# Kernel optimization log

Measured on AMD Instinct MI355X. Metric: run time of the kernel, lower is better.

## Reference

```python
import jax, jax.numpy as jnp
import numpy as np

LOG2 = 0.6931471805599453

def logcosh(x):
    # numerically stable log(cosh(x)) = |x| + log1p(exp(-2|x|)) - log(2)
    ax = jnp.abs(x)
    return ax + jnp.log1p(jnp.exp(-2.0 * ax)) - LOG2

def setup_inputs() -> dict:
    key = jax.random.key(0)
    k1, k2, k3 = jax.random.split(key, 3)
    B, N, G, F = 16384, 1024, 256, 16  # batch, n_sites, n_symm, alpha_symm
    # each row of perms is a valid permutation of [0, N)
    perms = jax.vmap(lambda k: jax.random.permutation(k, N))(jax.random.split(k1, G)).astype(jnp.int32)
    x = jax.random.normal(k2, (B, N), dtype=jnp.float32)
    W = jax.random.normal(k3, (N, F), dtype=jnp.float32) * 0.1  # kernel_init = normal(0.1)
    b = jnp.zeros((F,), dtype=jnp.float32)
    v_bias = jnp.zeros((1,), dtype=jnp.float32)
    return {"x": x, "W": W, "b": b, "v_bias": v_bias, "perms": perms}

def reference(x, W, b, v_bias, perms):
    # scan over group permutations: gather x by perm, matmul, bias, logcosh, sum
    def f(carry, perm):
        y = x[..., perm] @ W + b          # [B, F]
        return carry + jnp.sum(logcosh(y), axis=-1), None
    y0 = jnp.zeros(x.shape[:-1], dtype=x.dtype)
    y_out, _ = jax.lax.scan(f, y0, perms)
    y_out = y_out + v_bias[0] * jnp.sum(x, axis=-1)
    return y_out
```

## Files before the change

kernel.cpp:

```cpp
#include <hip/hip_runtime.h>
#include <math.h>

typedef __bf16 bf16x8 __attribute__((ext_vector_type(8)));
typedef float f32x4 __attribute__((ext_vector_type(4)));


__device__ __forceinline__ unsigned short f2bf(float f) {
    unsigned int u = __float_as_uint(f);
    u += 0x7FFFu + ((u >> 16) & 1u);
    return (unsigned short)(u >> 16);
}

__device__ __forceinline__ float logcosh_fast(float v) {
    float a = fabsf(v);
    float t = __expf(-2.0f * a);
    return a + (__logf(1.0f + t) - 0.6931471805599453f);
}

template <int CTRL>
__device__ __forceinline__ float dppadd(float x) {
    int y = __builtin_amdgcn_update_dpp(0, __float_as_int(x), CTRL, 0xf, 0xf, true);
    return x + __int_as_float(y);
}

__device__ __forceinline__ void gload_lds16(const void* g, void* l) {
    __builtin_amdgcn_global_load_lds(
        (__attribute__((address_space(1))) void*)(void*)g,
        (__attribute__((address_space(3))) void*)l, 16, 0, 0);
}

#define SBAR()  __builtin_amdgcn_s_barrier()
#define SCHED() __builtin_amdgcn_sched_barrier(0)

__global__ __launch_bounds__(256) void k_invert(const int* __restrict__ perms,
                                                int* __restrict__ inv) {
    int t = blockIdx.x * 256 + threadIdx.x;
    int g = t >> 10, n = t & 1023;
    inv[(g << 10) + perms[t]] = n;
}

__global__ __launch_bounds__(256) void k_build_bt(const float* __restrict__ W,
                                                  const int* __restrict__ inv,
                                                  unsigned short* __restrict__ bT) {
    int j = blockIdx.x;
    int g = j >> 4, f = j & 15;
    const int* invg = inv + (g << 10);
    size_t rowbase = (size_t)j << 10;
#pragma unroll
    for (int i = 0; i < 4; ++i) {
        int k = (i << 8) + threadIdx.x;
        int n = invg[k];
        bT[rowbase + k] = f2bf(W[(n << 4) + f]);
    }
}

__global__ __launch_bounds__(256) void k_convert(const float* __restrict__ x,
                                                 const float* __restrict__ vb,
                                                 unsigned short* __restrict__ xb,
                                                 float* __restrict__ out) {
    int row = blockIdx.x, tid = threadIdx.x;
    size_t base = ((size_t)row << 10) + (tid << 2);
    float4 v = *reinterpret_cast<const float4*>(x + base);
    ushort4 h;
    h.x = f2bf(v.x); h.y = f2bf(v.y); h.z = f2bf(v.z); h.w = f2bf(v.w);
    *reinterpret_cast<ushort4*>(xb + base) = h;
    float s = v.x + v.y + v.z + v.w;
#pragma unroll
    for (int off = 32; off > 0; off >>= 1) s += __shfl_down(s, off);
    __shared__ float ls[4];
    if ((tid & 63) == 0) ls[tid >> 6] = s;
    __syncthreads();
    if (tid == 0) out[row] = vb[0] * (ls[0] + ls[1] + ls[2] + ls[3]);
}


#define MFMA_M(MM)                                                               \
    _Pragma("unroll") for (int k_ = 0; k_ < 2; ++k_)                             \
    _Pragma("unroll") for (int n_ = 0; n_ < 4; ++n_)                             \
        acc[MM][n_] = __builtin_amdgcn_mfma_f32_16x16x32_bf16(                   \
            aF[MM][k_], bF[n_][k_], acc[MM][n_], 0, 0, 0);

__device__ __forceinline__ void stage_half(unsigned short* dst,
                                           const unsigned short* src, int h,
                                           int tid, int wv) {
#pragma unroll
    for (int j = 0; j < 2; ++j) {
        int c0 = (h * 128 + j * 64) * 8;
        int cc = c0 + tid;
        int r = cc >> 3;
        int cs = (cc & 7) ^ (r & 7);
        gload_lds16(src + (((size_t)r) << 10) + (cs << 3),
                    dst + ((c0 + wv * 64) << 3));
    }
}

template <bool STAGE, int VM>
__device__ __forceinline__ void tile_iter(
    const unsigned short* Ap, const unsigned short* Bp,
    unsigned short* AsD, unsigned short* BsD,
    const unsigned short* xsrc, const unsigned short* bsrc,
    f32x4 (&acc)[8][4], int aRow, int bRow, int po0, int po1, int tid, int wv) {
    bf16x8 aF[8][2], bF[4][2];

#pragma unroll
    for (int n = 0; n < 4; ++n) {
        bF[n][0] = *reinterpret_cast<const bf16x8*>(Bp + bRow + po0 + n * 1024);
        bF[n][1] = *reinterpret_cast<const bf16x8*>(Bp + bRow + po1 + n * 1024);
    }
#pragma unroll
    for (int m = 0; m < 2; ++m) {
        aF[m][0] = *reinterpret_cast<const bf16x8*>(Ap + aRow + po0 + m * 1024);
        aF[m][1] = *reinterpret_cast<const bf16x8*>(Ap + aRow + po1 + m * 1024);
    }
    SCHED();

#pragma unroll
    for (int m = 0; m < 6; ++m) {
        aF[m + 2][0] = *reinterpret_cast<const bf16x8*>(Ap + aRow + po0 + (m + 2) * 1024);
        aF[m + 2][1] = *reinterpret_cast<const bf16x8*>(Ap + aRow + po1 + (m + 2) * 1024);
        SCHED();
        asm volatile("s_waitcnt lgkmcnt(4)" ::: "memory");
        SCHED();
        __builtin_amdgcn_s_setprio(1);
        MFMA_M(m)
        __builtin_amdgcn_s_setprio(0);
        SCHED();
    }

    asm volatile("s_waitcnt lgkmcnt(0)" ::: "memory");
    SCHED();
    SBAR();

    if (STAGE) { stage_half(AsD, xsrc, 0, tid, wv); stage_half(AsD, xsrc, 1, tid, wv); }
    SCHED();
    __builtin_amdgcn_s_setprio(1);
    MFMA_M(6)
    __builtin_amdgcn_s_setprio(0);
    SCHED();

    if (STAGE) { stage_half(BsD, bsrc, 0, tid, wv); stage_half(BsD, bsrc, 1, tid, wv); }
    SCHED();
    __builtin_amdgcn_s_setprio(1);
    MFMA_M(7)
    __builtin_amdgcn_s_setprio(0);
    SCHED();
    if (VM == 8)      { asm volatile("s_waitcnt vmcnt(8)" ::: "memory"); }
    else if (VM == 0) { asm volatile("s_waitcnt vmcnt(0)" ::: "memory"); }
    SCHED();
    SBAR();
}

__global__ __launch_bounds__(512, 2) void k_gemm(const unsigned short* __restrict__ xb,
                                                 const unsigned short* __restrict__ bT,
                                                 const float* __restrict__ bias,
                                                 float* __restrict__ partial, int B) {
    __shared__ unsigned short As[2][256 * 64];
    __shared__ unsigned short Bs[2][256 * 64];

    const int tid = threadIdx.x;
    const int lane = tid & 63;
    const int wv = tid >> 6;
    const int wm = wv >> 2;
    const int wn = wv & 3;
    const int lr = lane & 15;
    const int lk = lane >> 4;

    const int fid = blockIdx.y * gridDim.x + blockIdx.x;
    const int cpx = (gridDim.x * gridDim.y) >> 3;
    const int swz = (fid & 7) * cpx + (fid >> 3);
    const int cbx = swz & 15;
    const int row0 = (swz >> 4) << 8;
    const int j0 = cbx << 8;

    const unsigned short* xbase = xb + ((size_t)row0 << 10);
    const unsigned short* bbase = bT + ((size_t)j0 << 10);

    const int aRow = (wm * 128 + lr) * 64;
    const int bRow = (wn * 64 + lr) * 64;
    const int po0 = (lk ^ (lr & 7)) * 8;
    const int po1 = ((4 + lk) ^ (lr & 7)) * 8;

    f32x4 acc[8][4];
#pragma unroll
    for (int m = 0; m < 8; ++m)
#pragma unroll
        for (int n = 0; n < 4; ++n)
            acc[m][n] = {0.f, 0.f, 0.f, 0.f};

    stage_half(&As[0][0], xbase, 0, tid, wv);
    stage_half(&As[0][0], xbase, 1, tid, wv);
    stage_half(&Bs[0][0], bbase, 0, tid, wv);
    stage_half(&Bs[0][0], bbase, 1, tid, wv);
    stage_half(&As[1][0], xbase + 64, 0, tid, wv);
    stage_half(&As[1][0], xbase + 64, 1, tid, wv);
    stage_half(&Bs[1][0], bbase + 64, 0, tid, wv);
    stage_half(&Bs[1][0], bbase + 64, 1, tid, wv);
    asm volatile("s_waitcnt vmcnt(8)" ::: "memory");
    SCHED();
    SBAR();

    for (int tt = 0; tt < 7; ++tt) {
        const int t0 = tt * 2;
        tile_iter<true, 8>(&As[0][0], &Bs[0][0], &As[0][0], &Bs[0][0],
                           xbase + ((t0 + 2) << 6), bbase + ((t0 + 2) << 6),
                           acc, aRow, bRow, po0, po1, tid, wv);
        tile_iter<true, 8>(&As[1][0], &Bs[1][0], &As[1][0], &Bs[1][0],
                           xbase + ((t0 + 3) << 6), bbase + ((t0 + 3) << 6),
                           acc, aRow, bRow, po0, po1, tid, wv);
    }
    tile_iter<false, 0>(&As[0][0], &Bs[0][0], &As[0][0], &Bs[0][0],
                        xbase, bbase, acc, aRow, bRow, po0, po1, tid, wv);
    tile_iter<false, -1>(&As[1][0], &Bs[1][0], &As[1][0], &Bs[1][0],
                         xbase, bbase, acc, aRow, bRow, po0, po1, tid, wv);

    float* rowsum = (float*)&As[0][0];
    const float bv = bias[lr];
#pragma unroll
    for (int m = 0; m < 8; ++m) {
#pragma unroll
        for (int r = 0; r < 4; ++r) {
            float s = 0.f;
#pragma unroll
            for (int n = 0; n < 4; ++n) s += logcosh_fast(acc[m][n][r] + bv);
            s = dppadd<0x111>(s);
            s = dppadd<0x112>(s);
            s = dppadd<0x114>(s);
            s = dppadd<0x118>(s);
            if (lr == 15)
                rowsum[wn * 256 + wm * 128 + m * 16 + lk * 4 + r] = s;
        }
    }
    __syncthreads();
    if (tid < 256) {
        float s = rowsum[tid] + rowsum[256 + tid] + rowsum[512 + tid] + rowsum[768 + tid];
        partial[(size_t)cbx * B + row0 + tid] = s;
    }
}

__global__ __launch_bounds__(256) void k_final(const float* __restrict__ partial,
                                               float* __restrict__ out, int ncb, int B) {
    int b = blockIdx.x * 256 + threadIdx.x;
    float s = out[b];
    for (int c = 0; c < ncb; ++c) s += partial[(size_t)c * B + b];
    out[b] = s;
}

extern "C" void kernel_launch(void* const* d_in, const int* in_sizes, int n_in,
                              void* d_out, int out_size, void* d_ws, size_t ws_size,
                              hipStream_t stream) {
    const float* x      = (const float*)d_in[0];
    const float* W      = (const float*)d_in[1];
    const float* bias   = (const float*)d_in[2];
    const float* v_bias = (const float*)d_in[3];
    const int*   perms  = (const int*)d_in[4];
    float* out = (float*)d_out;

    const int N  = 1024;
    const int B  = in_sizes[0] / N;
    const int G  = in_sizes[4] / N;
    const int GF = G * 16;
    const int NCB = GF / 256;

    char* w = (char*)d_ws;
    unsigned short* xb = (unsigned short*)w;
    unsigned short* bT = (unsigned short*)(w + (size_t)B * N * 2);
    int* inv = (int*)(w + (size_t)B * N * 2 + (size_t)GF * N * 2);
    float* partial = (float*)(w + (size_t)B * N * 2 + (size_t)GF * N * 2
                              + (size_t)G * N * 4);

    k_invert<<<G * N / 256, 256, 0, stream>>>(perms, inv);
    k_build_bt<<<GF, 256, 0, stream>>>(W, inv, bT);
    k_convert<<<B, 256, 0, stream>>>(x, v_bias, xb, out);
    k_gemm<<<dim3(NCB, B / 256), 512, 0, stream>>>(xb, bT, bias, partial, B);
    k_final<<<B / 256, 256, 0, stream>>>(partial, out, NCB, B);
}
```

Before: 188.4 us.

## Load B fragments directly to registers and drop LDS staging for B

```diff
diff --git a/kernel.cpp b/kernel.cpp
--- a/kernel.cpp
+++ b/kernel.cpp
@@ -74,77 +74,74 @@
 }
 
 
-#define MFMA_M(MM)                                                               \
-    _Pragma("unroll") for (int k_ = 0; k_ < 2; ++k_)                             \
+#define MFMA_M(MM, AFR)                                                          \
+    _Pragma("unroll") for (int kk_ = 0; kk_ < 2; ++kk_)                          \
     _Pragma("unroll") for (int n_ = 0; n_ < 4; ++n_)                             \
         acc[MM][n_] = __builtin_amdgcn_mfma_f32_16x16x32_bf16(                   \
-            aF[MM][k_], bF[n_][k_], acc[MM][n_], 0, 0, 0);
-
-__device__ __forceinline__ void stage_half(unsigned short* dst,
-                                           const unsigned short* src, int h,
-                                           int tid, int wv) {
-#pragma unroll
-    for (int j = 0; j < 2; ++j) {
-        int c0 = (h * 128 + j * 64) * 8;
-        int cc = c0 + tid;
-        int r = cc >> 3;
-        int cs = (cc & 7) ^ (r & 7);
-        gload_lds16(src + (((size_t)r) << 10) + (cs << 3),
-                    dst + ((c0 + wv * 64) << 3));
-    }
-}
-
-template <bool STAGE, int VM>
-__device__ __forceinline__ void tile_iter(
-    const unsigned short* Ap, const unsigned short* Bp,
-    unsigned short* AsD, unsigned short* BsD,
-    const unsigned short* xsrc, const unsigned short* bsrc,
-    f32x4 (&acc)[8][4], int aRow, int bRow, int po0, int po1, int tid, int wv) {
-    bf16x8 aF[8][2], bF[4][2];
-
-#pragma unroll
-    for (int n = 0; n < 4; ++n) {
-        bF[n][0] = *reinterpret_cast<const bf16x8*>(Bp + bRow + po0 + n * 1024);
-        bF[n][1] = *reinterpret_cast<const bf16x8*>(Bp + bRow + po1 + n * 1024);
-    }
+            AFR[kk_], bF[n_][kk_], acc[MM][n_], 0, 0, 0);
+
+__device__ __forceinline__ void stage_i(unsigned short* dst, const unsigned short* src,
+                                        int voff, int i, int wv) {
+    gload_lds16(src + voff, dst + (((i << 9) + wv * 64) << 3));
+}
+
+template <bool STA, bool LDB, int VM>
+__device__ __forceinline__ void tile_mw(
+    const unsigned short* Ap,
+    unsigned short* Adst,
+    const unsigned short* xsrc,
+    const unsigned short* bcol,
+    int ktN,
+    bf16x8 (&bF)[4][2],
+    f32x4 (&acc)[8][4],
+    const int (&vs)[4], int aRow, int po0, int po1, int wv) {
+    bf16x8 aF[4][2];
+
 #pragma unroll
     for (int m = 0; m < 2; ++m) {
         aF[m][0] = *reinterpret_cast<const bf16x8*>(Ap + aRow + po0 + m * 1024);
         aF[m][1] = *reinterpret_cast<const bf16x8*>(Ap + aRow + po1 + m * 1024);
     }
     SCHED();
-
 #pragma unroll
     for (int m = 0; m < 6; ++m) {
-        aF[m + 2][0] = *reinterpret_cast<const bf16x8*>(Ap + aRow + po0 + (m + 2) * 1024);
-        aF[m + 2][1] = *reinterpret_cast<const bf16x8*>(Ap + aRow + po1 + (m + 2) * 1024);
+        aF[(m + 2) & 3][0] = *reinterpret_cast<const bf16x8*>(Ap + aRow + po0 + (m + 2) * 1024);
+        aF[(m + 2) & 3][1] = *reinterpret_cast<const bf16x8*>(Ap + aRow + po1 + (m + 2) * 1024);
         SCHED();
         asm volatile("s_waitcnt lgkmcnt(4)" ::: "memory");
         SCHED();
         __builtin_amdgcn_s_setprio(1);
-        MFMA_M(m)
+        MFMA_M(m, aF[m & 3])
         __builtin_amdgcn_s_setprio(0);
         SCHED();
     }
-
     asm volatile("s_waitcnt lgkmcnt(0)" ::: "memory");
     SCHED();
     SBAR();
 
-    if (STAGE) { stage_half(AsD, xsrc, 0, tid, wv); stage_half(AsD, xsrc, 1, tid, wv); }
+    if (STA) {
+#pragma unroll
+        for (int i = 0; i < 4; ++i) stage_i(Adst, xsrc, vs[i], i, wv);
+    }
     SCHED();
     __builtin_amdgcn_s_setprio(1);
-    MFMA_M(6)
+    MFMA_M(6, aF[2])
     __builtin_amdgcn_s_setprio(0);
     SCHED();
 
-    if (STAGE) { stage_half(BsD, bsrc, 0, tid, wv); stage_half(BsD, bsrc, 1, tid, wv); }
-    SCHED();
     __builtin_amdgcn_s_setprio(1);
-    MFMA_M(7)
+    MFMA_M(7, aF[3])
     __builtin_amdgcn_s_setprio(0);
     SCHED();
-    if (VM == 8)      { asm volatile("s_waitcnt vmcnt(8)" ::: "memory"); }
+    if (LDB) {
+#pragma unroll
+        for (int n = 0; n < 4; ++n) {
+            bF[n][0] = *reinterpret_cast<const bf16x8*>(bcol + ktN + n * 16384);
+            bF[n][1] = *reinterpret_cast<const bf16x8*>(bcol + ktN + n * 16384 + 32);
+        }
+    }
+    SCHED();
+    if (VM == 12)     { asm volatile("s_waitcnt vmcnt(12)" ::: "memory"); }
     else if (VM == 0) { asm volatile("s_waitcnt vmcnt(0)" ::: "memory"); }
     SCHED();
     SBAR();
@@ -155,7 +152,6 @@
                                                  const float* __restrict__ bias,
                                                  float* __restrict__ partial, int B) {
     __shared__ unsigned short As[2][256 * 64];
-    __shared__ unsigned short Bs[2][256 * 64];
 
     const int tid = threadIdx.x;
     const int lane = tid & 63;
@@ -168,18 +164,27 @@
     const int fid = blockIdx.y * gridDim.x + blockIdx.x;
     const int cpx = (gridDim.x * gridDim.y) >> 3;
     const int swz = (fid & 7) * cpx + (fid >> 3);
-    const int cbx = swz & 15;
-    const int row0 = (swz >> 4) << 8;
+    const int rowb = swz & 63;
+    const int cbx = swz >> 6;
+    const int row0 = rowb << 8;
     const int j0 = cbx << 8;
 
     const unsigned short* xbase = xb + ((size_t)row0 << 10);
-    const unsigned short* bbase = bT + ((size_t)j0 << 10);
+    const unsigned short* bcol = bT + (((size_t)(j0 + wn * 64 + lr)) << 10) + lk * 8;
 
     const int aRow = (wm * 128 + lr) * 64;
-    const int bRow = (wn * 64 + lr) * 64;
     const int po0 = (lk ^ (lr & 7)) * 8;
     const int po1 = ((4 + lk) ^ (lr & 7)) * 8;
 
+    int vs[4];
+#pragma unroll
+    for (int i = 0; i < 4; ++i) {
+        int cc = (i << 9) + tid;
+        int r = cc >> 3;
+        int cs = (cc & 7) ^ (r & 7);
+        vs[i] = (r << 10) + (cs << 3);
+    }
+
     f32x4 acc[8][4];
 #pragma unroll
     for (int m = 0; m < 8; ++m)
@@ -187,31 +192,39 @@
         for (int n = 0; n < 4; ++n)
             acc[m][n] = {0.f, 0.f, 0.f, 0.f};
 
-    stage_half(&As[0][0], xbase, 0, tid, wv);
-    stage_half(&As[0][0], xbase, 1, tid, wv);
-    stage_half(&Bs[0][0], bbase, 0, tid, wv);
-    stage_half(&Bs[0][0], bbase, 1, tid, wv);
-    stage_half(&As[1][0], xbase + 64, 0, tid, wv);
-    stage_half(&As[1][0], xbase + 64, 1, tid, wv);
-    stage_half(&Bs[1][0], bbase + 64, 0, tid, wv);
-    stage_half(&Bs[1][0], bbase + 64, 1, tid, wv);
-    asm volatile("s_waitcnt vmcnt(8)" ::: "memory");
+    bf16x8 bF0[4][2], bF1[4][2];
+
+#pragma unroll
+    for (int i = 0; i < 4; ++i) stage_i(&As[0][0], xbase, vs[i], i, wv);
+#pragma unroll
+    for (int n = 0; n < 4; ++n) {
+        bF0[n][0] = *reinterpret_cast<const bf16x8*>(bcol + n * 16384);
+        bF0[n][1] = *reinterpret_cast<const bf16x8*>(bcol + n * 16384 + 32);
+    }
+#pragma unroll
+    for (int i = 0; i < 4; ++i) stage_i(&As[1][0], xbase + 64, vs[i], i, wv);
+#pragma unroll
+    for (int n = 0; n < 4; ++n) {
+        bF1[n][0] = *reinterpret_cast<const bf16x8*>(bcol + 64 + n * 16384);
+        bF1[n][1] = *reinterpret_cast<const bf16x8*>(bcol + 64 + n * 16384 + 32);
+    }
+    asm volatile("s_waitcnt vmcnt(12)" ::: "memory");
     SCHED();
     SBAR();
 
     for (int tt = 0; tt < 7; ++tt) {
         const int t0 = tt * 2;
-        tile_iter<true, 8>(&As[0][0], &Bs[0][0], &As[0][0], &Bs[0][0],
-                           xbase + ((t0 + 2) << 6), bbase + ((t0 + 2) << 6),
-                           acc, aRow, bRow, po0, po1, tid, wv);
-        tile_iter<true, 8>(&As[1][0], &Bs[1][0], &As[1][0], &Bs[1][0],
-                           xbase + ((t0 + 3) << 6), bbase + ((t0 + 3) << 6),
-                           acc, aRow, bRow, po0, po1, tid, wv);
-    }
-    tile_iter<false, 0>(&As[0][0], &Bs[0][0], &As[0][0], &Bs[0][0],
-                        xbase, bbase, acc, aRow, bRow, po0, po1, tid, wv);
-    tile_iter<false, -1>(&As[1][0], &Bs[1][0], &As[1][0], &Bs[1][0],
-                         xbase, bbase, acc, aRow, bRow, po0, po1, tid, wv);
+        tile_mw<true, true, 12>(&As[0][0], &As[0][0], xbase + ((t0 + 2) << 6),
+                                bcol, (t0 + 2) << 6,
+                                bF0, acc, vs, aRow, po0, po1, wv);
+        tile_mw<true, true, 12>(&As[1][0], &As[1][0], xbase + ((t0 + 3) << 6),
+                                bcol, (t0 + 3) << 6,
+                                bF1, acc, vs, aRow, po0, po1, wv);
+    }
+    tile_mw<false, false, 0>(&As[0][0], &As[0][0], xbase, bcol, 0,
+                             bF0, acc, vs, aRow, po0, po1, wv);
+    tile_mw<false, false, -1>(&As[1][0], &As[1][0], xbase, bcol, 0,
+                              bF1, acc, vs, aRow, po0, po1, wv);
 
     float* rowsum = (float*)&As[0][0];
     const float bv = bias[lr];
```

Result: slower. 246.1 us (+30.6%).

## Shrink GEMM block tile to 128x128 with 256 threads and higher occupancy

Applied to the files above, without the earlier changes.

```diff
diff --git a/kernel.cpp b/kernel.cpp
--- a/kernel.cpp
+++ b/kernel.cpp
@@ -75,32 +75,24 @@
 
 
 #define MFMA_M(MM)                                                               \
-    _Pragma("unroll") for (int k_ = 0; k_ < 2; ++k_)                             \
+    _Pragma("unroll") for (int kk_ = 0; kk_ < 2; ++kk_)                          \
     _Pragma("unroll") for (int n_ = 0; n_ < 4; ++n_)                             \
         acc[MM][n_] = __builtin_amdgcn_mfma_f32_16x16x32_bf16(                   \
-            aF[MM][k_], bF[n_][k_], acc[MM][n_], 0, 0, 0);
-
-__device__ __forceinline__ void stage_half(unsigned short* dst,
-                                           const unsigned short* src, int h,
-                                           int tid, int wv) {
-#pragma unroll
-    for (int j = 0; j < 2; ++j) {
-        int c0 = (h * 128 + j * 64) * 8;
-        int cc = c0 + tid;
-        int r = cc >> 3;
-        int cs = (cc & 7) ^ (r & 7);
-        gload_lds16(src + (((size_t)r) << 10) + (cs << 3),
-                    dst + ((c0 + wv * 64) << 3));
-    }
-}
-
-template <bool STAGE, int VM>
-__device__ __forceinline__ void tile_iter(
+            aF[MM][kk_], bF[n_][kk_], acc[MM][n_], 0, 0, 0);
+
+__device__ __forceinline__ void stage128(unsigned short* dst, const unsigned short* src,
+                                         int voff, int i, int wv) {
+    gload_lds16(src + voff, dst + (((i << 8) + (wv << 6)) << 3));
+}
+
+template <bool ST, int VM>
+__device__ __forceinline__ void tile128(
     const unsigned short* Ap, const unsigned short* Bp,
-    unsigned short* AsD, unsigned short* BsD,
+    unsigned short* Adst, unsigned short* Bdst,
     const unsigned short* xsrc, const unsigned short* bsrc,
-    f32x4 (&acc)[8][4], int aRow, int bRow, int po0, int po1, int tid, int wv) {
-    bf16x8 aF[8][2], bF[4][2];
+    f32x4 (&acc)[4][4], const int (&vs)[4],
+    int aRow, int bRow, int po0, int po1, int wv) {
+    bf16x8 aF[4][2], bF[4][2];
 
 #pragma unroll
     for (int n = 0; n < 4; ++n) {
@@ -113,36 +105,44 @@
         aF[m][1] = *reinterpret_cast<const bf16x8*>(Ap + aRow + po1 + m * 1024);
     }
     SCHED();
-
-#pragma unroll
-    for (int m = 0; m < 6; ++m) {
-        aF[m + 2][0] = *reinterpret_cast<const bf16x8*>(Ap + aRow + po0 + (m + 2) * 1024);
-        aF[m + 2][1] = *reinterpret_cast<const bf16x8*>(Ap + aRow + po1 + (m + 2) * 1024);
-        SCHED();
-        asm volatile("s_waitcnt lgkmcnt(4)" ::: "memory");
-        SCHED();
-        __builtin_amdgcn_s_setprio(1);
-        MFMA_M(m)
-        __builtin_amdgcn_s_setprio(0);
-        SCHED();
-    }
-
+    aF[2][0] = *reinterpret_cast<const bf16x8*>(Ap + aRow + po0 + 2 * 1024);
+    aF[2][1] = *reinterpret_cast<const bf16x8*>(Ap + aRow + po1 + 2 * 1024);
+    SCHED();
+    asm volatile("s_waitcnt lgkmcnt(4)" ::: "memory");
+    SCHED();
+    __builtin_amdgcn_s_setprio(1);
+    MFMA_M(0)
+    __builtin_amdgcn_s_setprio(0);
+    SCHED();
+    aF[3][0] = *reinterpret_cast<const bf16x8*>(Ap + aRow + po0 + 3 * 1024);
+    aF[3][1] = *reinterpret_cast<const bf16x8*>(Ap + aRow + po1 + 3 * 1024);
+    SCHED();
+    asm volatile("s_waitcnt lgkmcnt(4)" ::: "memory");
+    SCHED();
+    __builtin_amdgcn_s_setprio(1);
+    MFMA_M(1)
+    __builtin_amdgcn_s_setprio(0);
+    SCHED();
+    asm volatile("s_waitcnt lgkmcnt(2)" ::: "memory");
+    SCHED();
+    __builtin_amdgcn_s_setprio(1);
+    MFMA_M(2)
+    __builtin_amdgcn_s_setprio(0);
+    SCHED();
     asm volatile("s_waitcnt lgkmcnt(0)" ::: "memory");
     SCHED();
+    __builtin_amdgcn_s_setprio(1);
+    MFMA_M(3)
+    __builtin_amdgcn_s_setprio(0);
+    SCHED();
     SBAR();
 
-    if (STAGE) { stage_half(AsD, xsrc, 0, tid, wv); stage_half(AsD, xsrc, 1, tid, wv); }
-    SCHED();
-    __builtin_amdgcn_s_setprio(1);
-    MFMA_M(6)
-    __builtin_amdgcn_s_setprio(0);
-    SCHED();
-
-    if (STAGE) { stage_half(BsD, bsrc, 0, tid, wv); stage_half(BsD, bsrc, 1, tid, wv); }
-    SCHED();
-    __builtin_amdgcn_s_setprio(1);
-    MFMA_M(7)
-    __builtin_amdgcn_s_setprio(0);
+    if (ST) {
+#pragma unroll
+        for (int i = 0; i < 4; ++i) stage128(Adst, xsrc, vs[i], i, wv);
+#pragma unroll
+        for (int i = 0; i < 4; ++i) stage128(Bdst, bsrc, vs[i], i, wv);
+    }
     SCHED();
     if (VM == 8)      { asm volatile("s_waitcnt vmcnt(8)" ::: "memory"); }
     else if (VM == 0) { asm volatile("s_waitcnt vmcnt(0)" ::: "memory"); }
@@ -150,73 +150,83 @@
     SBAR();
 }
 
-__global__ __launch_bounds__(512, 2) void k_gemm(const unsigned short* __restrict__ xb,
+__global__ __launch_bounds__(256, 4) void k_gemm(const unsigned short* __restrict__ xb,
                                                  const unsigned short* __restrict__ bT,
                                                  const float* __restrict__ bias,
                                                  float* __restrict__ partial, int B) {
-    __shared__ unsigned short As[2][256 * 64];
-    __shared__ unsigned short Bs[2][256 * 64];
+    __shared__ unsigned short As[2][128 * 64];
+    __shared__ unsigned short Bs[2][128 * 64];
 
     const int tid = threadIdx.x;
     const int lane = tid & 63;
     const int wv = tid >> 6;
-    const int wm = wv >> 2;
-    const int wn = wv & 3;
+    const int wm = wv >> 1;
+    const int wn = wv & 1;
     const int lr = lane & 15;
     const int lk = lane >> 4;
 
     const int fid = blockIdx.y * gridDim.x + blockIdx.x;
     const int cpx = (gridDim.x * gridDim.y) >> 3;
     const int swz = (fid & 7) * cpx + (fid >> 3);
-    const int cbx = swz & 15;
-    const int row0 = (swz >> 4) << 8;
-    const int j0 = cbx << 8;
+    const int rowb = swz & 127;
+    const int cbx = swz >> 7;
+    const int row0 = rowb << 7;
+    const int j0 = cbx << 7;
 
     const unsigned short* xbase = xb + ((size_t)row0 << 10);
     const unsigned short* bbase = bT + ((size_t)j0 << 10);
 
-    const int aRow = (wm * 128 + lr) * 64;
+    const int aRow = (wm * 64 + lr) * 64;
     const int bRow = (wn * 64 + lr) * 64;
     const int po0 = (lk ^ (lr & 7)) * 8;
     const int po1 = ((4 + lk) ^ (lr & 7)) * 8;
 
-    f32x4 acc[8][4];
-#pragma unroll
-    for (int m = 0; m < 8; ++m)
+    int vs[4];
+#pragma unroll
+    for (int i = 0; i < 4; ++i) {
+        int cc = (i << 8) + tid;
+        int r = cc >> 3;
+        int cs = (cc & 7) ^ (r & 7);
+        vs[i] = (r << 10) + (cs << 3);
+    }
+
+    f32x4 acc[4][4];
+#pragma unroll
+    for (int m = 0; m < 4; ++m)
 #pragma unroll
         for (int n = 0; n < 4; ++n)
             acc[m][n] = {0.f, 0.f, 0.f, 0.f};
 
-    stage_half(&As[0][0], xbase, 0, tid, wv);
-    stage_half(&As[0][0], xbase, 1, tid, wv);
-    stage_half(&Bs[0][0], bbase, 0, tid, wv);
-    stage_half(&Bs[0][0], bbase, 1, tid, wv);
-    stage_half(&As[1][0], xbase + 64, 0, tid, wv);
-    stage_half(&As[1][0], xbase + 64, 1, tid, wv);
-    stage_half(&Bs[1][0], bbase + 64, 0, tid, wv);
-    stage_half(&Bs[1][0], bbase + 64, 1, tid, wv);
+#pragma unroll
+    for (int i = 0; i < 4; ++i) stage128(&As[0][0], xbase, vs[i], i, wv);
+#pragma unroll
+    for (int i = 0; i < 4; ++i) stage128(&Bs[0][0], bbase, vs[i], i, wv);
+#pragma unroll
+    for (int i = 0; i < 4; ++i) stage128(&As[1][0], xbase + 64, vs[i], i, wv);
+#pragma unroll
+    for (int i = 0; i < 4; ++i) stage128(&Bs[1][0], bbase + 64, vs[i], i, wv);
     asm volatile("s_waitcnt vmcnt(8)" ::: "memory");
     SCHED();
     SBAR();
 
     for (int tt = 0; tt < 7; ++tt) {
         const int t0 = tt * 2;
-        tile_iter<true, 8>(&As[0][0], &Bs[0][0], &As[0][0], &Bs[0][0],
-                           xbase + ((t0 + 2) << 6), bbase + ((t0 + 2) << 6),
-                           acc, aRow, bRow, po0, po1, tid, wv);
-        tile_iter<true, 8>(&As[1][0], &Bs[1][0], &As[1][0], &Bs[1][0],
-                           xbase + ((t0 + 3) << 6), bbase + ((t0 + 3) << 6),
-                           acc, aRow, bRow, po0, po1, tid, wv);
-    }
-    tile_iter<false, 0>(&As[0][0], &Bs[0][0], &As[0][0], &Bs[0][0],
-                        xbase, bbase, acc, aRow, bRow, po0, po1, tid, wv);
-    tile_iter<false, -1>(&As[1][0], &Bs[1][0], &As[1][0], &Bs[1][0],
-                         xbase, bbase, acc, aRow, bRow, po0, po1, tid, wv);
+        tile128<true, 8>(&As[0][0], &Bs[0][0], &As[0][0], &Bs[0][0],
+                         xbase + ((t0 + 2) << 6), bbase + ((t0 + 2) << 6),
+                         acc, vs, aRow, bRow, po0, po1, wv);
+        tile128<true, 8>(&As[1][0], &Bs[1][0], &As[1][0], &Bs[1][0],
+                         xbase + ((t0 + 3) << 6), bbase + ((t0 + 3) << 6),
+                         acc, vs, aRow, bRow, po0, po1, wv);
+    }
+    tile128<false, 0>(&As[0][0], &Bs[0][0], &As[0][0], &Bs[0][0],
+                      xbase, bbase, acc, vs, aRow, bRow, po0, po1, wv);
+    tile128<false, -1>(&As[1][0], &Bs[1][0], &As[1][0], &Bs[1][0],
+                       xbase, bbase, acc, vs, aRow, bRow, po0, po1, wv);
 
     float* rowsum = (float*)&As[0][0];
     const float bv = bias[lr];
 #pragma unroll
-    for (int m = 0; m < 8; ++m) {
+    for (int m = 0; m < 4; ++m) {
 #pragma unroll
         for (int r = 0; r < 4; ++r) {
             float s = 0.f;
@@ -227,14 +237,12 @@
             s = dppadd<0x114>(s);
             s = dppadd<0x118>(s);
             if (lr == 15)
-                rowsum[wn * 256 + wm * 128 + m * 16 + lk * 4 + r] = s;
+                rowsum[wn * 128 + wm * 64 + m * 16 + lk * 4 + r] = s;
         }
     }
     __syncthreads();
-    if (tid < 256) {
-        float s = rowsum[tid] + rowsum[256 + tid] + rowsum[512 + tid] + rowsum[768 + tid];
-        partial[(size_t)cbx * B + row0 + tid] = s;
-    }
+    if (tid < 128)
+        partial[(size_t)cbx * B + row0 + tid] = rowsum[tid] + rowsum[128 + tid];
 }
 
 __global__ __launch_bounds__(256) void k_final(const float* __restrict__ partial,
@@ -259,7 +267,7 @@
     const int B  = in_sizes[0] / N;
     const int G  = in_sizes[4] / N;
     const int GF = G * 16;
-    const int NCB = GF / 256;
+    const int NCB = GF / 128;
 
     char* w = (char*)d_ws;
     unsigned short* xb = (unsigned short*)w;
@@ -271,6 +279,6 @@
     k_invert<<<G * N / 256, 256, 0, stream>>>(perms, inv);
     k_build_bt<<<GF, 256, 0, stream>>>(W, inv, bT);
     k_convert<<<B, 256, 0, stream>>>(x, v_bias, xb, out);
-    k_gemm<<<dim3(NCB, B / 256), 512, 0, stream>>>(xb, bT, bias, partial, B);
+    k_gemm<<<dim3(NCB, B / 128), 256, 0, stream>>>(xb, bT, bias, partial, B);
     k_final<<<B / 256, 256, 0, stream>>>(partial, out, NCB, B);
 }
```

New measurement: 221.8 us. 1.18x slower.

## Make GEMM persistent over four row tiles with cross-tile prefetch and direct partial stores

Applied to the files above, without the earlier changes.

```diff
diff --git a/kernel.cpp b/kernel.cpp
--- a/kernel.cpp
+++ b/kernel.cpp
@@ -80,18 +80,9 @@
         acc[MM][n_] = __builtin_amdgcn_mfma_f32_16x16x32_bf16(                   \
             aF[MM][k_], bF[n_][k_], acc[MM][n_], 0, 0, 0);
 
-__device__ __forceinline__ void stage_half(unsigned short* dst,
-                                           const unsigned short* src, int h,
-                                           int tid, int wv) {
-#pragma unroll
-    for (int j = 0; j < 2; ++j) {
-        int c0 = (h * 128 + j * 64) * 8;
-        int cc = c0 + tid;
-        int r = cc >> 3;
-        int cs = (cc & 7) ^ (r & 7);
-        gload_lds16(src + (((size_t)r) << 10) + (cs << 3),
-                    dst + ((c0 + wv * 64) << 3));
-    }
+__device__ __forceinline__ void stage_i(unsigned short* dst, const unsigned short* src,
+                                        int voff, int i, int wv) {
+    gload_lds16(src + voff, dst + (((i << 9) + (wv << 6)) << 3));
 }
 
 template <bool STAGE, int VM>
@@ -99,7 +90,8 @@
     const unsigned short* Ap, const unsigned short* Bp,
     unsigned short* AsD, unsigned short* BsD,
     const unsigned short* xsrc, const unsigned short* bsrc,
-    f32x4 (&acc)[8][4], int aRow, int bRow, int po0, int po1, int tid, int wv) {
+    f32x4 (&acc)[8][4], const int (&vs)[4],
+    int aRow, int bRow, int po0, int po1, int wv) {
     bf16x8 aF[8][2], bF[4][2];
 
 #pragma unroll
@@ -131,14 +123,20 @@
     SCHED();
     SBAR();
 
-    if (STAGE) { stage_half(AsD, xsrc, 0, tid, wv); stage_half(AsD, xsrc, 1, tid, wv); }
+    if (STAGE) {
+#pragma unroll
+        for (int i = 0; i < 4; ++i) stage_i(AsD, xsrc, vs[i], i, wv);
+    }
     SCHED();
     __builtin_amdgcn_s_setprio(1);
     MFMA_M(6)
     __builtin_amdgcn_s_setprio(0);
     SCHED();
 
-    if (STAGE) { stage_half(BsD, bsrc, 0, tid, wv); stage_half(BsD, bsrc, 1, tid, wv); }
+    if (STAGE) {
+#pragma unroll
+        for (int i = 0; i < 4; ++i) stage_i(BsD, bsrc, vs[i], i, wv);
+    }
     SCHED();
     __builtin_amdgcn_s_setprio(1);
     MFMA_M(7)
@@ -165,21 +163,30 @@
     const int lr = lane & 15;
     const int lk = lane >> 4;
 
-    const int fid = blockIdx.y * gridDim.x + blockIdx.x;
-    const int cpx = (gridDim.x * gridDim.y) >> 3;
-    const int swz = (fid & 7) * cpx + (fid >> 3);
-    const int cbx = swz & 15;
-    const int row0 = (swz >> 4) << 8;
+    const int bid = blockIdx.x;
+    const int x8 = bid & 7, u = bid >> 3;
+    const int cbx = (x8 & 3) * 4 + (u & 3);
+    const int chain = (x8 >> 2) * 8 + (u >> 2);
     const int j0 = cbx << 8;
 
-    const unsigned short* xbase = xb + ((size_t)row0 << 10);
     const unsigned short* bbase = bT + ((size_t)j0 << 10);
+    const unsigned short* xcur = xb + ((size_t)(chain << 10) << 10);
+    const unsigned short* xnext = xcur + (256 << 10);
 
     const int aRow = (wm * 128 + lr) * 64;
     const int bRow = (wn * 64 + lr) * 64;
     const int po0 = (lk ^ (lr & 7)) * 8;
     const int po1 = ((4 + lk) ^ (lr & 7)) * 8;
 
+    int vs[4];
+#pragma unroll
+    for (int i = 0; i < 4; ++i) {
+        int cc = (i << 9) + tid;
+        int r = cc >> 3;
+        int cs = (cc & 7) ^ (r & 7);
+        vs[i] = (r << 10) + (cs << 3);
+    }
+
     f32x4 acc[8][4];
 #pragma unroll
     for (int m = 0; m < 8; ++m)
@@ -187,61 +194,82 @@
         for (int n = 0; n < 4; ++n)
             acc[m][n] = {0.f, 0.f, 0.f, 0.f};
 
-    stage_half(&As[0][0], xbase, 0, tid, wv);
-    stage_half(&As[0][0], xbase, 1, tid, wv);
-    stage_half(&Bs[0][0], bbase, 0, tid, wv);
-    stage_half(&Bs[0][0], bbase, 1, tid, wv);
-    stage_half(&As[1][0], xbase + 64, 0, tid, wv);
-    stage_half(&As[1][0], xbase + 64, 1, tid, wv);
-    stage_half(&Bs[1][0], bbase + 64, 0, tid, wv);
-    stage_half(&Bs[1][0], bbase + 64, 1, tid, wv);
+#pragma unroll
+    for (int i = 0; i < 4; ++i) stage_i(&As[0][0], xcur, vs[i], i, wv);
+#pragma unroll
+    for (int i = 0; i < 4; ++i) stage_i(&Bs[0][0], bbase, vs[i], i, wv);
+#pragma unroll
+    for (int i = 0; i < 4; ++i) stage_i(&As[1][0], xcur + 64, vs[i], i, wv);
+#pragma unroll
+    for (int i = 0; i < 4; ++i) stage_i(&Bs[1][0], bbase + 64, vs[i], i, wv);
     asm volatile("s_waitcnt vmcnt(8)" ::: "memory");
     SCHED();
     SBAR();
 
-    for (int tt = 0; tt < 7; ++tt) {
-        const int t0 = tt * 2;
-        tile_iter<true, 8>(&As[0][0], &Bs[0][0], &As[0][0], &Bs[0][0],
-                           xbase + ((t0 + 2) << 6), bbase + ((t0 + 2) << 6),
-                           acc, aRow, bRow, po0, po1, tid, wv);
-        tile_iter<true, 8>(&As[1][0], &Bs[1][0], &As[1][0], &Bs[1][0],
-                           xbase + ((t0 + 3) << 6), bbase + ((t0 + 3) << 6),
-                           acc, aRow, bRow, po0, po1, tid, wv);
-    }
-    tile_iter<false, 0>(&As[0][0], &Bs[0][0], &As[0][0], &Bs[0][0],
-                        xbase, bbase, acc, aRow, bRow, po0, po1, tid, wv);
-    tile_iter<false, -1>(&As[1][0], &Bs[1][0], &As[1][0], &Bs[1][0],
-                         xbase, bbase, acc, aRow, bRow, po0, po1, tid, wv);
-
-    float* rowsum = (float*)&As[0][0];
     const float bv = bias[lr];
-#pragma unroll
-    for (int m = 0; m < 8; ++m) {
-#pragma unroll
-        for (int r = 0; r < 4; ++r) {
-            float s = 0.f;
-#pragma unroll
-            for (int n = 0; n < 4; ++n) s += logcosh_fast(acc[m][n][r] + bv);
-            s = dppadd<0x111>(s);
-            s = dppadd<0x112>(s);
-            s = dppadd<0x114>(s);
-            s = dppadd<0x118>(s);
-            if (lr == 15)
-                rowsum[wn * 256 + wm * 128 + m * 16 + lk * 4 + r] = s;
+    int row0 = chain << 10;
+
+    for (int p = 0; p < 4; ++p) {
+        const bool last = (p == 3);
+
+        for (int tt = 0; tt < 7; ++tt) {
+            const int t0 = tt * 2;
+            tile_iter<true, 8>(&As[0][0], &Bs[0][0], &As[0][0], &Bs[0][0],
+                               xcur + ((t0 + 2) << 6), bbase + ((t0 + 2) << 6),
+                               acc, vs, aRow, bRow, po0, po1, wv);
+            tile_iter<true, 8>(&As[1][0], &Bs[1][0], &As[1][0], &Bs[1][0],
+                               xcur + ((t0 + 3) << 6), bbase + ((t0 + 3) << 6),
+                               acc, vs, aRow, bRow, po0, po1, wv);
         }
-    }
-    __syncthreads();
-    if (tid < 256) {
-        float s = rowsum[tid] + rowsum[256 + tid] + rowsum[512 + tid] + rowsum[768 + tid];
-        partial[(size_t)cbx * B + row0 + tid] = s;
+        if (!last) {
+            tile_iter<true, 8>(&As[0][0], &Bs[0][0], &As[0][0], &Bs[0][0],
+                               xnext, bbase, acc, vs, aRow, bRow, po0, po1, wv);
+            tile_iter<true, 8>(&As[1][0], &Bs[1][0], &As[1][0], &Bs[1][0],
+                               xnext + 64, bbase + 64, acc, vs, aRow, bRow, po0, po1, wv);
+        } else {
+            tile_iter<false, 0>(&As[0][0], &Bs[0][0], &As[0][0], &Bs[0][0],
+                                xcur, bbase, acc, vs, aRow, bRow, po0, po1, wv);
+            tile_iter<false, -1>(&As[1][0], &Bs[1][0], &As[1][0], &Bs[1][0],
+                                 xcur, bbase, acc, vs, aRow, bRow, po0, po1, wv);
+        }
+
+        {
+            float* pdst = partial + (size_t)(cbx * 4 + wn) * B + row0 + wm * 128;
+#pragma unroll
+            for (int m = 0; m < 8; ++m) {
+                f32x4 sv;
+#pragma unroll
+                for (int r = 0; r < 4; ++r) {
+                    float s = 0.f;
+#pragma unroll
+                    for (int n = 0; n < 4; ++n) s += logcosh_fast(acc[m][n][r] + bv);
+                    s = dppadd<0x111>(s);
+                    s = dppadd<0x112>(s);
+                    s = dppadd<0x114>(s);
+                    s = dppadd<0x118>(s);
+                    sv[r] = s;
+                }
+                if (lr == 15)
+                    *reinterpret_cast<f32x4*>(pdst + m * 16 + lk * 4) = sv;
+            }
+        }
+#pragma unroll
+        for (int m = 0; m < 8; ++m)
+#pragma unroll
+            for (int n = 0; n < 4; ++n)
+                acc[m][n] = {0.f, 0.f, 0.f, 0.f};
+
+        xcur = xnext;
+        xnext += (256 << 10);
+        row0 += 256;
     }
 }
 
 __global__ __launch_bounds__(256) void k_final(const float* __restrict__ partial,
-                                               float* __restrict__ out, int ncb, int B) {
+                                               float* __restrict__ out, int ns, int B) {
     int b = blockIdx.x * 256 + threadIdx.x;
     float s = out[b];
-    for (int c = 0; c < ncb; ++c) s += partial[(size_t)c * B + b];
+    for (int c = 0; c < ns; ++c) s += partial[(size_t)c * B + b];
     out[b] = s;
 }
 
@@ -259,7 +287,7 @@
     const int B  = in_sizes[0] / N;
     const int G  = in_sizes[4] / N;
     const int GF = G * 16;
-    const int NCB = GF / 256;
+    const int NS = (GF / 256) * 4;
 
     char* w = (char*)d_ws;
     unsigned short* xb = (unsigned short*)w;
@@ -271,6 +299,6 @@
     k_invert<<<G * N / 256, 256, 0, stream>>>(perms, inv);
     k_build_bt<<<GF, 256, 0, stream>>>(W, inv, bT);
     k_convert<<<B, 256, 0, stream>>>(x, v_bias, xb, out);
-    k_gemm<<<dim3(NCB, B / 256), 512, 0, stream>>>(xb, bT, bias, partial, B);
-    k_final<<<B / 256, 256, 0, stream>>>(partial, out, NCB, B);
-}
+    k_gemm<<<256, 512, 0, stream>>>(xb, bT, bias, partial, B);
+    k_final<<<B / 256, 256, 0, stream>>>(partial, out, NS, B);
+}
```

Measured after the change: 356.0 us. 1.89x slower.
